# Performance work log

Hardware: AMD Instinct MI355X
Metric: run time of the kernel (lower is better)

## Reference

```python
import jax, jax.numpy as jnp
import numpy as np


def setup_inputs() -> dict:
    key = jax.random.key(0)
    k1, k2 = jax.random.split(key)
    B, L, D = 16, 512, 256
    text_features = jax.random.normal(k1, (B, L, D), dtype=jnp.float32)
    durations = jax.random.randint(k2, (B, L), 0, 32, dtype=jnp.int64)
    return {"text_features": text_features, "durations": durations, "target_length": 8192}


def reference(text_features, durations, target_length):
    """Length-regulator: expand [B,L,d] phoneme features to [B,T,d] frames.

    Frame t of batch b copies phoneme p where cumsum(dur)[b,p-1] <= t < cumsum(dur)[b,p];
    frames past the total duration are zero (matches torch zeros-init + trim/pad to
    target_length, since padding with the last frame only occurs when the buffer was
    already target_length long in the original code path with target_length set).
    """
    B, L, D = text_features.shape
    T = target_length  # static python int -> jit-friendly fixed output length
    cum = jnp.cumsum(durations, axis=1)                      # [B, L]
    t = jnp.arange(T, dtype=cum.dtype)                       # [T]
    # first phoneme index p with cum[b,p] > t  (side='right')
    idx = jax.vmap(lambda c: jnp.searchsorted(c, t, side='right'))(cum)  # [B, T]
    idx = jnp.minimum(idx, L - 1)
    valid = t[None, :] < cum[:, -1:]                         # [B, T] frames within total dur
    gathered = jnp.take_along_axis(text_features, idx[:, :, None], axis=1)  # [B, T, D]
    return jnp.where(valid[:, :, None], gathered, jnp.zeros((), dtype=text_features.dtype))
```

## Files before the change

### kernel.cpp

```cpp
#include <hip/hip_runtime.h>

#define MAX_L 2048
#define MAX_EPC 8
#define FPB 128

__global__ __launch_bounds__(256) void lr_fused_kernel(
        const float* __restrict__ feat,
        const int* __restrict__ dur,
        const int* __restrict__ tlen,
        float* __restrict__ out,
        int BL, int BT, int D) {
    const int T = *tlen;
    const int B = BT / T;
    const int L = BL / B;
    const int vecs = D >> 2;

    __shared__ int sc[MAX_L];
    __shared__ int swsum[4];
    __shared__ int sidx[FPB];

    const long frame_base0 = (long)blockIdx.x * FPB;
    if (frame_base0 >= BT) return;

    const int tid  = threadIdx.x;
    const int lane = tid & 63;
    const int wv   = tid >> 6;

    long fb_ = frame_base0;
    int remaining = (int)((long)BT - frame_base0 < FPB ? (long)BT - frame_base0
                                                       : (long)FPB);

    while (remaining > 0) {
        const int b   = (int)(fb_ / T);
        const int tt0 = (int)(fb_ - (long)b * T);
        const int seg = remaining < (T - tt0) ? remaining : (T - tt0);

        __syncthreads();
        const int epc  = (L + blockDim.x - 1) / blockDim.x;
        const int base = tid * epc;
        const int* __restrict__ drow = dur + (size_t)b * L;
        int local[MAX_EPC];
        int run = 0;
#pragma unroll
        for (int e = 0; e < MAX_EPC; ++e) {
            int v = 0;
            if (e < epc && base + e < L) v = drow[base + e];
            run += v;
            local[e] = run;
        }
        int wsum = run;
#pragma unroll
        for (int off = 1; off < 64; off <<= 1) {
            int up = __shfl_up(wsum, off, 64);
            if (lane >= off) wsum += up;
        }
        if (lane == 63) swsum[wv] = wsum;
        __syncthreads();
        int wprefix = 0;
        for (int w = 0; w < wv; ++w) wprefix += swsum[w];
        const int chunk_prefix = wprefix + wsum - run;
#pragma unroll
        for (int e = 0; e < MAX_EPC; ++e)
            if (e < epc && base + e < L) sc[base + e] = chunk_prefix + local[e];
        __syncthreads();

        const int total = sc[L - 1];

        if (tid < seg) {
            const int t = tt0 + tid;
            int p = -1;
            if (t < total) {
                int lo = 0, hi = L - 1;
                while (lo < hi) {
                    const int mid = (lo + hi) >> 1;
                    if (sc[mid] > t) hi = mid;
                    else             lo = mid + 1;
                }
                p = lo;
            }
            sidx[tid] = p;
        }
        __syncthreads();

        if (seg == FPB && vecs == 64) {
            const float4* __restrict__ fbp =
                (const float4*)feat + (size_t)b * L * 64;
            float4* __restrict__ op =
                (float4*)out + ((size_t)fb_ + (size_t)wv * 32) * 64 + lane;
            const int si = sidx[wv * 32 + (lane & 31)];
            int prev = -2;
            float4 v = make_float4(0.f, 0.f, 0.f, 0.f);
#pragma unroll
            for (int j = 0; j < 32; ++j) {
                const int p = __builtin_amdgcn_readlane(si, j);
                if (p != prev) {
                    v = (p >= 0) ? fbp[(size_t)p * 64 + lane]
                                 : make_float4(0.f, 0.f, 0.f, 0.f);
                    prev = p;
                }
                op[(size_t)j * 64] = v;
            }
        } else {
            const float4* __restrict__ fbp =
                (const float4*)feat + (size_t)b * L * vecs;
            const float4 z = make_float4(0.f, 0.f, 0.f, 0.f);
            for (int f = wv; f < seg; f += 4) {
                const int p = sidx[f];
                float4* __restrict__ orow = (float4*)out + ((size_t)fb_ + f) * vecs;
                if (p >= 0) {
                    const float4* __restrict__ irow = fbp + (size_t)p * vecs;
                    for (int i = lane; i < vecs; i += 64) orow[i] = irow[i];
                } else {
                    for (int i = lane; i < vecs; i += 64) orow[i] = z;
                }
            }
        }

        fb_ += seg;
        remaining -= seg;
    }
}

extern "C" void kernel_launch(void* const* d_in, const int* in_sizes, int n_in,
                              void* d_out, int out_size, void* d_ws, size_t ws_size,
                              hipStream_t stream) {
    const float* feat = (const float*)d_in[0];
    const int*   dur  = (const int*)d_in[1];
    const int*   tlen = (const int*)d_in[2];

    const int BL = in_sizes[1];
    const int D  = in_sizes[0] / in_sizes[1];
    const int BT = out_size / D;

    const int grid = (BT + FPB - 1) / FPB;
    lr_fused_kernel<<<grid, 256, 0, stream>>>(feat, dur, tlen, (float*)d_out,
                                              BL, BT, D);
}
```

Baseline: 144.9 us.

## Stage contiguous phoneme rows in shared memory before scattering frames

Replaces the per-wave readlane gather loop with a block-cooperative scheme. The block loads up to 16 consecutive phoneme feature rows into LDS, finds via atomicMin how many frames those rows cover, and then writes those frames from LDS. Padding frames past the total duration are written as zeros in a separate loop. The aim is coalesced, deduplicated global reads, at the cost of extra __syncthreads per window and LDS round trips, which could serialize a kernel that is mostly bound by write bandwidth.

```diff
diff --git a/kernel.cpp b/kernel.cpp
--- a/kernel.cpp
+++ b/kernel.cpp
@@ -3,6 +3,7 @@
 #define MAX_L 2048
 #define MAX_EPC 8
 #define FPB 128
+#define ROWS 16
 
 __global__ __launch_bounds__(256) void lr_fused_kernel(
         const float* __restrict__ feat,
@@ -18,6 +19,8 @@
     __shared__ int sc[MAX_L];
     __shared__ int swsum[4];
     __shared__ int sidx[FPB];
+    __shared__ float4 srows[ROWS * 64];
+    __shared__ int sf2;
 
     const long frame_base0 = (long)blockIdx.x * FPB;
     if (frame_base0 >= BT) return;
@@ -27,8 +30,8 @@
     const int wv   = tid >> 6;
 
     long fb_ = frame_base0;
-    int remaining = (int)((long)BT - frame_base0 < FPB ? (long)BT - frame_base0
-                                                       : (long)FPB);
+    long rem_l = (long)BT - frame_base0;
+    int remaining = (int)(rem_l < FPB ? rem_l : (long)FPB);
 
     while (remaining > 0) {
         const int b   = (int)(fb_ / T);
@@ -82,31 +85,45 @@
         }
         __syncthreads();
 
-        if (seg == FPB && vecs == 64) {
-            const float4* __restrict__ fbp =
-                (const float4*)feat + (size_t)b * L * 64;
-            float4* __restrict__ op =
-                (float4*)out + ((size_t)fb_ + (size_t)wv * 32) * 64 + lane;
-            const int si = sidx[wv * 32 + (lane & 31)];
-            int prev = -2;
-            float4 v = make_float4(0.f, 0.f, 0.f, 0.f);
-#pragma unroll
-            for (int j = 0; j < 32; ++j) {
-                const int p = __builtin_amdgcn_readlane(si, j);
-                if (p != prev) {
-                    v = (p >= 0) ? fbp[(size_t)p * 64 + lane]
-                                 : make_float4(0.f, 0.f, 0.f, 0.f);
-                    prev = p;
+        int nvalid = total - tt0;
+        if (nvalid < 0) nvalid = 0;
+        if (nvalid > seg) nvalid = seg;
+
+        if (vecs == 64) {
+            int f = 0;
+            while (f < nvalid) {
+                const int w0 = sidx[f];
+                if (tid == 0) sf2 = nvalid;
+                __syncthreads();
+                if (tid > f && tid < nvalid && sidx[tid] >= w0 + ROWS)
+                    atomicMin(&sf2, tid);
+                int nr = L - w0; if (nr > ROWS) nr = ROWS;
+                const float4* __restrict__ fbp =
+                    (const float4*)feat + ((size_t)b * L + w0) * 64;
+                for (int i = tid; i < nr * 64; i += 256)
+                    srows[i] = fbp[i];
+                __syncthreads();
+                const int f2 = sf2;
+                float4* __restrict__ ob =
+                    (float4*)out + (size_t)fb_ * 64 + lane;
+                for (int j = f + wv; j < f2; j += 4) {
+                    const int r = sidx[j] - w0;
+                    const float4 v = srows[r * 64 + lane];
+                    ob[(size_t)j * 64] = v;
                 }
-                op[(size_t)j * 64] = v;
+                f = f2;
             }
+            const float4 z = make_float4(0.f, 0.f, 0.f, 0.f);
+            float4* __restrict__ ob = (float4*)out + (size_t)fb_ * 64 + lane;
+            for (int j = nvalid + wv; j < seg; j += 4)
+                ob[(size_t)j * 64] = z;
         } else {
             const float4* __restrict__ fbp =
                 (const float4*)feat + (size_t)b * L * vecs;
             const float4 z = make_float4(0.f, 0.f, 0.f, 0.f);
-            for (int f = wv; f < seg; f += 4) {
-                const int p = sidx[f];
-                float4* __restrict__ orow = (float4*)out + ((size_t)fb_ + f) * vecs;
+            for (int fj = wv; fj < seg; fj += 4) {
+                const int p = sidx[fj];
+                float4* __restrict__ orow = (float4*)out + ((size_t)fb_ + fj) * vecs;
                 if (p >= 0) {
                     const float4* __restrict__ irow = fbp + (size_t)p * vecs;
                     for (int i = lane; i < vecs; i += 64) orow[i] = irow[i];
```

After: 158.5 us. +9.4%, slower.
